# Kernel tuning notes

Hardware: AMD Instinct MI355X
Metric: run time of the kernel (lower is better)

## Reference

```python
import jax, jax.numpy as jnp
from jax import lax
import numpy as np

N_WORDS, SENT_LEN, N_HEADS = 8192, 64, 1024
INPUT_SIZE, HIDDEN, DIST_EMB, CONV_CH, MAX_DIST = 768, 1024, 64, 4, 128
L_MAX = SENT_LEN  # static max sentence length (uniform sentences in setup)


def setup_inputs():
    key = jax.random.key(0)
    ks = jax.random.split(key, 8)
    sent_id = (jnp.arange(N_WORDS) // SENT_LEN).astype(jnp.int32)
    words = jax.random.normal(ks[0], (N_WORDS, INPUT_SIZE), jnp.float32)
    heads_ids = jnp.sort(jax.random.randint(ks[1], (N_HEADS,), 0, N_WORDS)).astype(jnp.int32)
    in_dim = 2 * INPUT_SIZE + DIST_EMB
    def lin(k, i, o):
        return (jax.random.normal(k, (i, o), jnp.float32) / np.float32(np.sqrt(i)))
    return dict(
        sent_id=sent_id, words=words, heads_ids=heads_ids,
        W1=lin(ks[2], in_dim, HIDDEN), b1=jnp.zeros((HIDDEN,), jnp.float32),
        W2=lin(ks[3], HIDDEN, 256), b2=jnp.zeros((256,), jnp.float32),
        W3=lin(ks[4], 256, DIST_EMB), b3=jnp.zeros((DIST_EMB,), jnp.float32),
        conv1_w=jax.random.normal(ks[5], (CONV_CH, DIST_EMB, 3), jnp.float32) * 0.05,
        conv1_b=jnp.zeros((CONV_CH,), jnp.float32),
        conv2_w=jax.random.normal(ks[6], (2, CONV_CH, 3), jnp.float32) * 0.2,
        conv2_b=jnp.zeros((2,), jnp.float32),
        emb=jax.random.normal(ks[7], (MAX_DIST, DIST_EMB), jnp.float32),
    )


def _conv1d(x, w, b):
    # x: [N, C_in, L], w: [C_out, C_in, K=3]; padding=1 exactly as the torch module
    y = lax.conv_general_dilated(x, w, (1,), [(1, 1)],
                                 dimension_numbers=('NCH', 'OIH', 'NCH'))
    return y + b[None, :, None]


def reference(sent_id, words, heads_ids, W1, b1, W2, b2, W3, b3,
              conv1_w, conv1_b, conv2_w, conv2_b, emb):
    n_words = words.shape[0]
    n_heads = heads_ids.shape[0]
    md = emb.shape[0]
    heads = heads_ids.astype(jnp.int32)
    sid_h = sent_id[heads]
    # sent_id is sorted: each sentence is a contiguous run of words, so the
    # ragged nonzero(same_sent) cols for head h are start[h] .. start[h]+len[h]-1
    start = jnp.searchsorted(sent_id, sid_h, side='left')
    lengths = jnp.searchsorted(sent_id, sid_h, side='right') - start
    j = jnp.arange(L_MAX)
    cols = start[:, None] + j[None, :]                  # [H, L]
    valid = j[None, :] < lengths[:, None]               # padding_mask
    cols_c = jnp.minimum(cols, n_words - 1)
    rel = heads[:, None] - cols_c                       # relative positions
    emb_ids = rel + (md - 2) // 2
    emb_ids = jnp.where((emb_ids < 0) | (emb_ids > md - 2), md - 1, emb_ids)
    # padded pair matrix: [H, L, 2*input + dist_emb], zeros at padded slots
    pair = jnp.concatenate([
        jnp.broadcast_to(words[heads][:, None, :], (n_heads, L_MAX, words.shape[1])),
        words[cols_c],
        emb[emb_ids],
    ], axis=-1)
    pair = jnp.where(valid[..., None], pair, 0.0)
    # FFNN (eval mode: dropout = identity)
    h = jax.nn.relu(pair @ W1 + b1)
    h = jax.nn.relu(h @ W2 + b2)
    h = h @ W3 + b3                                     # [H, L, DIST_EMB]
    x = jnp.transpose(h, (0, 2, 1))                     # [H, C, L]
    x = _conv1d(x, conv1_w, conv1_b)
    x = _conv1d(x, conv2_w, conv2_b)
    res = jnp.transpose(x, (0, 2, 1))                   # [H, L, 2]
    # scatter valid entries back into a -inf-filled [H, n_words, 2] tensor
    scores = jnp.full((n_heads, n_words, 2), -jnp.inf, jnp.float32)
    rows = jnp.broadcast_to(jnp.arange(n_heads)[:, None], cols.shape)
    cols_sc = jnp.where(valid, cols, n_words)           # OOB index -> dropped
    scores = scores.at[rows, cols_sc].set(res, mode='drop')
    # eval-mode validity masks: starts must be <= head, ends >= head
    rel_full = heads[:, None] - jnp.arange(n_words)[None, :]
    valid_starts = jnp.where(rel_full >= 0, 0.0, -jnp.inf)
    valid_ends = jnp.where(rel_full <= 0, 0.0, -jnp.inf)
    return scores + jnp.stack([valid_starts, valid_ends], axis=2)
```

## Files before the change

kernel.cpp:

```cpp
#include <hip/hip_runtime.h>
#include <cstdint>
#include <cstddef>

#define NW   8192
#define NH   1024
#define INP  768
#define HID  1024
#define DE   64
#define LMAX 64

#define NEG_SENT (-3.0e38f)

typedef short bf16x8 __attribute__((ext_vector_type(8)));
typedef float f32x4  __attribute__((ext_vector_type(4)));

__device__ __forceinline__ unsigned short f2bf(float f) {
    unsigned u = __builtin_bit_cast(unsigned, f);
    u += 0x7FFFu + ((u >> 16) & 1u);
    return (unsigned short)(u >> 16);
}
__device__ __forceinline__ float bcf(unsigned u) {
    return __builtin_bit_cast(float, u);
}

__device__ __forceinline__ void gload_lds16(const void* g, void* lds) {
    __builtin_amdgcn_global_load_lds(
        (const __attribute__((address_space(1))) unsigned int*)g,
        (__attribute__((address_space(3))) unsigned int*)lds, 16, 0, 0);
}

__device__ __forceinline__ bf16x8 mk_af(uint4 u, uint4 v, uint4 e) {
    bf16x8 r;
    const unsigned* up = (const unsigned*)&u;
    const unsigned* vp = (const unsigned*)&v;
    const unsigned* ep = (const unsigned*)&e;
    unsigned* rp = (unsigned*)&r;
    #pragma unroll
    for (int q = 0; q < 4; ++q) {
        const unsigned ud = up[q], vd = vp[q], ed = ep[q];
        float slo = bcf(ud << 16) + bcf(vd << 16) + bcf(ed << 16);
        float shi = bcf(ud & 0xffff0000u) + bcf(vd & 0xffff0000u) + bcf(ed & 0xffff0000u);
        slo = fmaxf(slo, 0.f);
        shi = fmaxf(shi, 0.f);
        rp[q] = (unsigned)f2bf(slo) | ((unsigned)f2bf(shi) << 16);
    }
    return r;
}

__device__ __forceinline__ bf16x8 cvt8(float4 x, float4 y) {
    bf16x8 r;
    r[0] = (short)f2bf(x.x); r[1] = (short)f2bf(x.y);
    r[2] = (short)f2bf(x.z); r[3] = (short)f2bf(x.w);
    r[4] = (short)f2bf(y.x); r[5] = (short)f2bf(y.y);
    r[6] = (short)f2bf(y.z); r[7] = (short)f2bf(y.w);
    return r;
}

__device__ __forceinline__ void pack_frags_body(
    const float* __restrict__ src, uint4* __restrict__ dst,
    int Ntiles, int N, int t)
{
    const int frag = t >> 6, l = t & 63;
    const int kc = frag / Ntiles, nt = frag - kc * Ntiles;
    const int k0 = kc * 32 + ((l >> 4) << 3);
    const int n  = nt * 16 + (l & 15);
    unsigned wv[4];
    #pragma unroll
    for (int r = 0; r < 4; ++r) {
        const unsigned lo = f2bf(src[(size_t)(k0 + 2 * r)     * N + n]);
        const unsigned hi = f2bf(src[(size_t)(k0 + 2 * r + 1) * N + n]);
        wv[r] = lo | (hi << 16);
    }
    dst[t] = make_uint4(wv[0], wv[1], wv[2], wv[3]);
}

__global__ __launch_bounds__(256) void pack_all(
    const int* __restrict__ sent_id, const int* __restrict__ heads_ids,
    const float* __restrict__ W1, const float* __restrict__ b1,
    const float* __restrict__ W2, const float* __restrict__ W3,
    uint4* __restrict__ W2p, uint4* __restrict__ W3p,
    uint4* __restrict__ W1bp, uint4* __restrict__ W1ap,
    uint4* __restrict__ W1cp,
    unsigned short* __restrict__ b1b, unsigned short* __restrict__ zrow,
    int* __restrict__ hstart, int* __restrict__ hlen)
{
    const int b = blockIdx.x, tid = threadIdx.x;
    if (b < 4) {
        const int i = b * 256 + tid;
        b1b[i] = f2bf(b1[i]);
        zrow[i] = 0;
        const int head = heads_ids[i];
        const int sid = sent_id[head];
        int lo = 0, hi = NW;
        while (lo < hi) { int m = (lo + hi) >> 1; if (sent_id[m] < sid) lo = m + 1; else hi = m; }
        const int st = lo;
        int lo2 = lo, hi2 = NW;
        while (lo2 < hi2) { int m = (lo2 + hi2) >> 1; if (sent_id[m] <= sid) lo2 = m + 1; else hi2 = m; }
        int ln = lo2 - st;
        if (ln > LMAX) ln = LMAX;
        hstart[i] = st; hlen[i] = ln;
    }
    else if (b < 132)  pack_frags_body(W2, W2p, 16, 256, (b - 4) * 256 + tid);
    else if (b < 140)  pack_frags_body(W3, W3p, 4, 64, (b - 132) * 256 + tid);
    else if (b < 524)  pack_frags_body(W1 + (size_t)INP * HID, W1bp, 64, 1024, (b - 140) * 256 + tid);
    else if (b < 908)  pack_frags_body(W1, W1ap, 64, 1024, (b - 524) * 256 + tid);
    else               pack_frags_body(W1 + (size_t)2 * INP * HID, W1cp, 64, 1024, (b - 908) * 256 + tid);
}

__global__ __launch_bounds__(256) void gemm_vue(
    const float* __restrict__ words, const int* __restrict__ heads_ids,
    const float* __restrict__ emb,
    const uint4* __restrict__ W1bp, const uint4* __restrict__ W1ap,
    const uint4* __restrict__ W1cp, const float* __restrict__ b1,
    unsigned short* __restrict__ Vb, unsigned short* __restrict__ Ub,
    unsigned short* __restrict__ Eb)
{
    __shared__ char sbuf[2][16384];
    const int tid = threadIdx.x;
    const int l = tid & 63, wid = tid >> 6;

    const float* Asrc; const int* gather = nullptr;
    const uint4* Bp; unsigned short* Cb; const float* bias = nullptr;
    int Kc, by, bx, lda;
    {
        const int bid = blockIdx.x;
        if (bid < 512)      { Asrc = words; lda = INP; Bp = W1bp; Cb = Vb; Kc = 24; by = bid >> 3; bx = bid & 7; }
        else if (bid < 576) { const int bb = bid - 512; Asrc = words; lda = INP; gather = heads_ids; Bp = W1ap; Cb = Ub; bias = b1; Kc = 24; by = bb >> 3; bx = bb & 7; }
        else                { const int bb = bid - 576; Asrc = emb; lda = DE; Bp = W1cp; Cb = Eb; Kc = 2; by = 0; bx = bb; }
    }
    const int mt0 = by * 8, nt0 = bx * 8;
    const int NtTot = 64, N = 1024;
    const int wm = (wid >> 1) * 4, wn = (wid & 1) * 4;

    const float* arow[2]; int koffA[2];
    #pragma unroll
    for (int q = 0; q < 2; ++q) {
        const int e = tid + q * 256;
        const int f = e >> 6, ll2 = e & 63;
        int r = (mt0 + f) * 16 + (ll2 & 15);
        if (gather) r = gather[r];
        arow[q]  = Asrc + (size_t)r * lda;
        koffA[q] = (ll2 >> 4) << 3;
    }

    f32x4 acc[4][4];
    #pragma unroll
    for (int i = 0; i < 4; ++i)
        #pragma unroll
        for (int j = 0; j < 4; ++j) acc[i][j] = (f32x4){0.f, 0.f, 0.f, 0.f};

    float4 a0, a1, a2, a3;
    #define STAGE_A_LOAD(kc) do {                                          \
        a0 = *(const float4*)(arow[0] + (kc) * 32 + koffA[0]);             \
        a1 = *(const float4*)(arow[0] + (kc) * 32 + koffA[0] + 4);         \
        a2 = *(const float4*)(arow[1] + (kc) * 32 + koffA[1]);             \
        a3 = *(const float4*)(arow[1] + (kc) * 32 + koffA[1] + 4); } while (0)
    #define STAGE_B(kc, b) do {                                            \
        gload_lds16(Bp + ((size_t)(kc) * NtTot + nt0 + wid) * 64 + l,      \
                    sbuf[b] + 8192 + wid * 1024 + l * 16);                 \
        gload_lds16(Bp + ((size_t)(kc) * NtTot + nt0 + 4 + wid) * 64 + l,  \
                    sbuf[b] + 8192 + (4 + wid) * 1024 + l * 16); } while (0)
    #define STAGE_A_WRITE(b) do {                                          \
        *(bf16x8*)(sbuf[b] + tid * 16)         = cvt8(a0, a1);             \
        *(bf16x8*)(sbuf[b] + (tid + 256) * 16) = cvt8(a2, a3); } while (0)

    STAGE_A_LOAD(0);
    STAGE_B(0, 0);
    STAGE_A_WRITE(0);

    for (int kc = 0; kc < Kc; ++kc) {
        const int p = kc & 1;
        __builtin_amdgcn_s_barrier();
        if (kc + 1 < Kc) {
            STAGE_A_LOAD(kc + 1);
            STAGE_B(kc + 1, p ^ 1);
            STAGE_A_WRITE(p ^ 1);
            asm volatile("s_waitcnt vmcnt(2) lgkmcnt(0)" ::: "memory");
        } else {
            asm volatile("s_waitcnt vmcnt(0) lgkmcnt(0)" ::: "memory");
        }
        __builtin_amdgcn_s_barrier();
        bf16x8 af[4], bf[4];
        #pragma unroll
        for (int i = 0; i < 4; ++i)
            af[i] = *(const bf16x8*)(sbuf[p] + ((wm + i) * 64 + l) * 16);
        #pragma unroll
        for (int j = 0; j < 4; ++j)
            bf[j] = *(const bf16x8*)(sbuf[p] + 8192 + ((wn + j) * 64 + l) * 16);
        #pragma unroll
        for (int i = 0; i < 4; ++i)
            #pragma unroll
            for (int j = 0; j < 4; ++j)
                acc[i][j] = __builtin_amdgcn_mfma_f32_16x16x32_bf16(
                    af[i], bf[j], acc[i][j], 0, 0, 0);
    }
    #undef STAGE_A_LOAD
    #undef STAGE_B
    #undef STAGE_A_WRITE

    const int bm = mt0 * 16, bn = nt0 * 16;
    #pragma unroll
    for (int i = 0; i < 4; ++i)
        #pragma unroll
        for (int j = 0; j < 4; ++j) {
            const int row0 = bm + (wm + i) * 16 + ((l >> 4) << 2);
            const int col  = bn + (wn + j) * 16 + (l & 15);
            const float bv = bias ? bias[col] : 0.f;
            #pragma unroll
            for (int r = 0; r < 4; ++r)
                Cb[(size_t)(row0 + r) * N + col] = f2bf(acc[i][j][r] + bv);
        }
}

__global__ __launch_bounds__(256, 4) void head_kernel(
    const int* __restrict__ hstart, const int* __restrict__ hlen,
    const int* __restrict__ heads_ids,
    const unsigned short* __restrict__ Vb, const unsigned short* __restrict__ Ub,
    const unsigned short* __restrict__ Eb, const unsigned short* __restrict__ b1b,
    const unsigned short* __restrict__ zrow,
    const uint4* __restrict__ W2p, const float* __restrict__ b2,
    const uint4* __restrict__ W3p, const float* __restrict__ b3,
    const float* __restrict__ c1w, const float* __restrict__ c1b,
    const float* __restrict__ c2w, const float* __restrict__ c2b,
    float* __restrict__ out)
{
    __shared__ char smem[32768];
    const int h   = (blockIdx.x & 7) * 128 + (blockIdx.x >> 3);
    const int tid = threadIdx.x;
    const int w = tid >> 6, l = tid & 63;
    const int head  = heads_ids[h];
    const int start = hstart[h];
    const int len   = hlen[h];

    const int arow = w * 16 + (l & 15);
    const int g8   = (l >> 4) << 3;
    const bool valid = arow < len;
    const int wglob = start + arow;
    const int wc    = wglob < NW ? wglob : NW - 1;
    int eid = head - wc + 63;
    eid = (eid < 0 || eid > 126) ? 127 : eid;
    const unsigned short* Vp = valid ? Vb + (size_t)wc  * HID : zrow;
    const unsigned short* Ep = valid ? Eb + (size_t)eid * HID : zrow;

    if (tid < 128)
        *(uint4*)(smem + 8192 + tid * 16) = *(const uint4*)(Ub + (size_t)h * HID + tid * 8);
    else
        *(uint4*)(smem + 10240 + (tid - 128) * 16) = *(const uint4*)(b1b + (tid - 128) * 8);
    const char* ubase = smem + (valid ? 8192 : 10240);

    char* slot0 = smem;
    char* slot1 = smem + 4096;
    const uint4* WpB = W2p + (size_t)(w * 4) * 64 + l;

    f32x4 acc[16];
    #pragma unroll
    for (int i = 0; i < 16; ++i) acc[i] = (f32x4){0.f, 0.f, 0.f, 0.f};

    uint4 vX, eX, vY, eY;
    bf16x8 Ba0, Ba1, Ba2, Ba3;

    #define LOAD_VE(kc, vv, ee) do {                           \
        vv = *(const uint4*)(Vp + (kc) * 32 + g8);             \
        ee = *(const uint4*)(Ep + (kc) * 32 + g8); } while (0)
    #define LOAD_U(kc) (*(const uint4*)(ubase + (kc) * 64 + (g8 << 1)))
    #define LOAD_B(kc) do {                                    \
        const uint4* p_ = WpB + (size_t)(kc) * 16 * 64;        \
        Ba0 = *(const bf16x8*)(p_);                            \
        Ba1 = *(const bf16x8*)(p_ + 64);                       \
        Ba2 = *(const bf16x8*)(p_ + 128);                      \
        Ba3 = *(const bf16x8*)(p_ + 192); } while (0)
    #define CONSUME(slot) do {                                 \
        bf16x8 a0 = *(const bf16x8*)((slot) + 0 * 1024 + l * 16); \
        bf16x8 a1 = *(const bf16x8*)((slot) + 1 * 1024 + l * 16); \
        bf16x8 a2 = *(const bf16x8*)((slot) + 2 * 1024 + l * 16); \
        bf16x8 a3 = *(const bf16x8*)((slot) + 3 * 1024 + l * 16); \
        acc[0]  = __builtin_amdgcn_mfma_f32_16x16x32_bf16(a0, Ba0, acc[0],  0,0,0); \
        acc[1]  = __builtin_amdgcn_mfma_f32_16x16x32_bf16(a0, Ba1, acc[1],  0,0,0); \
        acc[2]  = __builtin_amdgcn_mfma_f32_16x16x32_bf16(a0, Ba2, acc[2],  0,0,0); \
        acc[3]  = __builtin_amdgcn_mfma_f32_16x16x32_bf16(a0, Ba3, acc[3],  0,0,0); \
        acc[4]  = __builtin_amdgcn_mfma_f32_16x16x32_bf16(a1, Ba0, acc[4],  0,0,0); \
        acc[5]  = __builtin_amdgcn_mfma_f32_16x16x32_bf16(a1, Ba1, acc[5],  0,0,0); \
        acc[6]  = __builtin_amdgcn_mfma_f32_16x16x32_bf16(a1, Ba2, acc[6],  0,0,0); \
        acc[7]  = __builtin_amdgcn_mfma_f32_16x16x32_bf16(a1, Ba3, acc[7],  0,0,0); \
        acc[8]  = __builtin_amdgcn_mfma_f32_16x16x32_bf16(a2, Ba0, acc[8],  0,0,0); \
        acc[9]  = __builtin_amdgcn_mfma_f32_16x16x32_bf16(a2, Ba1, acc[9],  0,0,0); \
        acc[10] = __builtin_amdgcn_mfma_f32_16x16x32_bf16(a2, Ba2, acc[10], 0,0,0); \
        acc[11] = __builtin_amdgcn_mfma_f32_16x16x32_bf16(a2, Ba3, acc[11], 0,0,0); \
        acc[12] = __builtin_amdgcn_mfma_f32_16x16x32_bf16(a3, Ba0, acc[12], 0,0,0); \
        acc[13] = __builtin_amdgcn_mfma_f32_16x16x32_bf16(a3, Ba1, acc[13], 0,0,0); \
        acc[14] = __builtin_amdgcn_mfma_f32_16x16x32_bf16(a3, Ba2, acc[14], 0,0,0); \
        acc[15] = __builtin_amdgcn_mfma_f32_16x16x32_bf16(a3, Ba3, acc[15], 0,0,0); } while (0)

    LOAD_VE(0, vX, eX);
    LOAD_VE(1, vY, eY);
    LOAD_B(0);
    __syncthreads();
    {
        bf16x8 af = mk_af(LOAD_U(0), vX, eX);
        *(bf16x8*)(slot0 + w * 1024 + l * 16) = af;
    }
    LOAD_VE(2, vX, eX);

    for (int kc = 0; kc < 32; kc += 2) {
        asm volatile("s_waitcnt lgkmcnt(0)" ::: "memory");
        __builtin_amdgcn_s_barrier();
        {
            bf16x8 af = mk_af(LOAD_U(kc + 1), vY, eY);
            *(bf16x8*)(slot1 + w * 1024 + l * 16) = af;
        }
        if (kc + 3 < 32) LOAD_VE(kc + 3, vY, eY);
        CONSUME(slot0);
        LOAD_B(kc + 1);
        asm volatile("s_waitcnt lgkmcnt(0)" ::: "memory");
        __builtin_amdgcn_s_barrier();
        if (kc + 2 < 32) {
            bf16x8 af = mk_af(LOAD_U(kc + 2), vX, eX);
            *(bf16x8*)(slot0 + w * 1024 + l * 16) = af;
        }
        if (kc + 4 < 32) LOAD_VE(kc + 4, vX, eX);
        CONSUME(slot1);
        if (kc + 2 < 32) LOAD_B(kc + 2);
    }
    #undef LOAD_VE
    #undef LOAD_U
    #undef LOAD_B
    #undef CONSUME

    __syncthreads();
    {
        float b2v[4];
        #pragma unroll
        for (int ntl = 0; ntl < 4; ++ntl) b2v[ntl] = b2[w * 64 + ntl * 16 + (l & 15)];
        #pragma unroll
        for (int mt = 0; mt < 4; ++mt)
            #pragma unroll
            for (int ntl = 0; ntl < 4; ++ntl) {
                const int n = w * 64 + ntl * 16 + (l & 15);
                #pragma unroll
                for (int r = 0; r < 4; ++r) {
                    const int m = mt * 16 + ((l >> 4) << 2) + r;
                    const float x = fmaxf(acc[mt * 4 + ntl][r] + b2v[ntl], 0.f);
                    *(unsigned short*)(smem + m * 512 + ((n * 2) ^ ((m & 7) << 4))) = f2bf(x);
                }
            }
    }
    __syncthreads();

    f32x4 acc3[4];
    #pragma unroll
    for (int i = 0; i < 4; ++i) acc3[i] = (f32x4){0.f, 0.f, 0.f, 0.f};
    const int mrow = w * 16 + (l & 15);
    #pragma unroll
    for (int kc = 0; kc < 8; ++kc) {
        const int n0 = kc * 32 + g8;
        const bf16x8 af = *(const bf16x8*)(smem + mrow * 512 + ((n0 * 2) ^ ((mrow & 7) << 4)));
        #pragma unroll
        for (int nt = 0; nt < 4; ++nt) {
            const bf16x8 bf = *(const bf16x8*)(W3p + (size_t)((kc << 2) + nt) * 64 + l);
            acc3[nt] = __builtin_amdgcn_mfma_f32_16x16x32_bf16(af, bf, acc3[nt], 0, 0, 0);
        }
    }
    __syncthreads();
    float* h3s = (float*)smem;
    float* o1  = (float*)(smem + 16640);
    #pragma unroll
    for (int nt = 0; nt < 4; ++nt) {
        const int c = nt * 16 + (l & 15);
        const float b3v = b3[c];
        #pragma unroll
        for (int r = 0; r < 4; ++r) {
            const int m = w * 16 + ((l >> 4) << 2) + r;
            h3s[m * 65 + c] = acc3[nt][r] + b3v;
        }
    }
    if (tid < 8) o1[(tid >> 1) * 66 + ((tid & 1) ? 65 : 0)] = 0.f;
    __syncthreads();

    {
        const int o = tid >> 6, ll = tid & 63;
        float a = c1b[o];
        #pragma unroll 8
        for (int cc = 0; cc < 64; ++cc) {
            const float w0  = c1w[o * 192 + cc * 3 + 0];
            const float w1  = c1w[o * 192 + cc * 3 + 1];
            const float w2v = c1w[o * 192 + cc * 3 + 2];
            if (ll > 0)  a += h3s[(ll - 1) * 65 + cc] * w0;
            a += h3s[ll * 65 + cc] * w1;
            if (ll < 63) a += h3s[(ll + 1) * 65 + cc] * w2v;
        }
        o1[o * 66 + ll + 1] = a;
    }
    __syncthreads();

    if (tid < 128) {
        const int s = tid >> 6, ll = tid & 63;
        float z = c2b[s];
        #pragma unroll
        for (int cc = 0; cc < 4; ++cc)
            #pragma unroll
            for (int k = 0; k < 3; ++k)
                z += o1[cc * 66 + ll + k] * c2w[s * 12 + cc * 3 + k];
        if (ll < len) {
            const int wv = start + ll;
            const bool ok = (s == 0) ? (wv <= head) : (wv >= head);
            out[(size_t)h * (NW * 2) + (size_t)wv * 2 + s] = ok ? z : NEG_SENT;
        }
    }

    {
        float4 ni; ni.x = NEG_SENT; ni.y = NEG_SENT; ni.z = NEG_SENT; ni.w = NEG_SENT;
        float4* orow = reinterpret_cast<float4*>(out + (size_t)h * (NW * 2));
        const int cA = start >> 1;
        const int cB = (start + len - 1) >> 1;
        for (int ch = tid; ch < NW / 2; ch += 256) {
            if (ch >= cA && ch <= cB) {
                #pragma unroll
                for (int t = 0; t < 2; ++t) {
                    const int wv = 2 * ch + t;
                    if (wv < start || wv >= start + len) {
                        out[(size_t)h * (NW * 2) + (size_t)wv * 2]     = NEG_SENT;
                        out[(size_t)h * (NW * 2) + (size_t)wv * 2 + 1] = NEG_SENT;
                    }
                }
            } else {
                orow[ch] = ni;
            }
        }
    }
}

extern "C" void kernel_launch(void* const* d_in, const int* in_sizes, int n_in,
                              void* d_out, int out_size, void* d_ws, size_t ws_size,
                              hipStream_t stream)
{
    const int*   sent_id = (const int*)  d_in[0];
    const float* words   = (const float*)d_in[1];
    const int*   heads   = (const int*)  d_in[2];
    const float* W1      = (const float*)d_in[3];
    const float* b1      = (const float*)d_in[4];
    const float* W2      = (const float*)d_in[5];
    const float* b2      = (const float*)d_in[6];
    const float* W3      = (const float*)d_in[7];
    const float* b3      = (const float*)d_in[8];
    const float* c1w     = (const float*)d_in[9];
    const float* c1b     = (const float*)d_in[10];
    const float* c2w     = (const float*)d_in[11];
    const float* c2b     = (const float*)d_in[12];
    const float* emb     = (const float*)d_in[13];
    float* out = (float*)d_out;

    uint4* W2p  = (uint4*)d_ws;
    uint4* W3p  = W2p  + 32 * 16 * 64;
    uint4* W1bp = W3p  + 8 * 4 * 64;
    uint4* W1ap = W1bp + 24 * 64 * 64;
    uint4* W1cp = W1ap + 24 * 64 * 64;
    unsigned short* Vb   = (unsigned short*)(W1cp + 2 * 64 * 64);
    unsigned short* Ub   = Vb + (size_t)NW * HID;
    unsigned short* Eb   = Ub + (size_t)NH * HID;
    unsigned short* b1b  = Eb + (size_t)128 * HID;
    unsigned short* zrow = b1b + HID;
    int* hstart = (int*)(zrow + HID);
    int* hlen   = hstart + NH;

    dim3 blk(256);
    pack_all<<<dim3(940), blk, 0, stream>>>(
        sent_id, heads, W1, b1, W2, W3,
        W2p, W3p, W1bp, W1ap, W1cp, b1b, zrow, hstart, hlen);
    gemm_vue<<<dim3(584), blk, 0, stream>>>(
        words, heads, emb, W1bp, W1ap, W1cp, b1, Vb, Ub, Eb);
    head_kernel<<<dim3(NH), blk, 0, stream>>>(
        hstart, hlen, heads, Vb, Ub, Eb, b1b, zrow,
        W2p, b2, W3p, b3, c1w, c1b, c2w, c2b, out);
}
```

Measured before the change: 227.8 us.

## Pre-pack activations to bf16 MFMA fragments and use hardware bf16 conversion

Moves the fp32-to-bf16 conversion of word, gathered-head and embedding rows out of the GEMM main loop into the packing kernel. Operands are written in MFMA fragment layout, so the GEMM can stream both A and B into LDS with direct global-to-LDS loads. Software round-to-nearest bf16 conversion is replaced everywhere by the v_cvt_pk_bf16_f32 instruction. In exchange it adds an extra full write and re-read of packed activations (about 12 MB of bf16 for words) through global memory, plus a larger pack launch.

Measured after the change: 211.3 us. 7.3% less time.

```diff
diff --git a/kernel.cpp b/kernel.cpp
--- a/kernel.cpp
+++ b/kernel.cpp
@@ -22,6 +22,11 @@
 __device__ __forceinline__ float bcf(unsigned u) {
     return __builtin_bit_cast(float, u);
 }
+__device__ __forceinline__ unsigned cvtpk(float a, float b) {
+    unsigned r;
+    asm("v_cvt_pk_bf16_f32 %0, %1, %2" : "=v"(r) : "v"(a), "v"(b));
+    return r;
+}
 
 __device__ __forceinline__ void gload_lds16(const void* g, void* lds) {
     __builtin_amdgcn_global_load_lds(
@@ -40,19 +45,8 @@
         const unsigned ud = up[q], vd = vp[q], ed = ep[q];
         float slo = bcf(ud << 16) + bcf(vd << 16) + bcf(ed << 16);
         float shi = bcf(ud & 0xffff0000u) + bcf(vd & 0xffff0000u) + bcf(ed & 0xffff0000u);
-        slo = fmaxf(slo, 0.f);
-        shi = fmaxf(shi, 0.f);
-        rp[q] = (unsigned)f2bf(slo) | ((unsigned)f2bf(shi) << 16);
-    }
-    return r;
-}
-
-__device__ __forceinline__ bf16x8 cvt8(float4 x, float4 y) {
-    bf16x8 r;
-    r[0] = (short)f2bf(x.x); r[1] = (short)f2bf(x.y);
-    r[2] = (short)f2bf(x.z); r[3] = (short)f2bf(x.w);
-    r[4] = (short)f2bf(y.x); r[5] = (short)f2bf(y.y);
-    r[6] = (short)f2bf(y.z); r[7] = (short)f2bf(y.w);
+        rp[q] = cvtpk(fmaxf(slo, 0.f), fmaxf(shi, 0.f));
+    }
     return r;
 }
 
@@ -66,11 +60,26 @@
     const int n  = nt * 16 + (l & 15);
     unsigned wv[4];
     #pragma unroll
-    for (int r = 0; r < 4; ++r) {
-        const unsigned lo = f2bf(src[(size_t)(k0 + 2 * r)     * N + n]);
-        const unsigned hi = f2bf(src[(size_t)(k0 + 2 * r + 1) * N + n]);
-        wv[r] = lo | (hi << 16);
-    }
+    for (int r = 0; r < 4; ++r)
+        wv[r] = cvtpk(src[(size_t)(k0 + 2 * r) * N + n],
+                      src[(size_t)(k0 + 2 * r + 1) * N + n]);
+    dst[t] = make_uint4(wv[0], wv[1], wv[2], wv[3]);
+}
+
+__device__ __forceinline__ void pack_rows_body(
+    const float* __restrict__ src, uint4* __restrict__ dst,
+    const int* __restrict__ gather, int Kc, int ldsrc, int t)
+{
+    const int l = t & 63, frag = t >> 6;
+    const int mt = frag / Kc, kc = frag - mt * Kc;
+    int row = mt * 16 + (l & 15);
+    if (gather) row = gather[row];
+    const int k0 = kc * 32 + ((l >> 4) << 3);
+    const float* s = src + (size_t)row * ldsrc + k0;
+    unsigned wv[4];
+    #pragma unroll
+    for (int r = 0; r < 4; ++r)
+        wv[r] = cvtpk(s[2 * r], s[2 * r + 1]);
     dst[t] = make_uint4(wv[0], wv[1], wv[2], wv[3]);
 }
 
@@ -78,9 +87,11 @@
     const int* __restrict__ sent_id, const int* __restrict__ heads_ids,
     const float* __restrict__ W1, const float* __restrict__ b1,
     const float* __restrict__ W2, const float* __restrict__ W3,
+    const float* __restrict__ words, const float* __restrict__ emb,
     uint4* __restrict__ W2p, uint4* __restrict__ W3p,
     uint4* __restrict__ W1bp, uint4* __restrict__ W1ap,
-    uint4* __restrict__ W1cp,
+    uint4* __restrict__ W1cp, uint4* __restrict__ Ep_a,
+    uint4* __restrict__ Awp, uint4* __restrict__ Aup,
     unsigned short* __restrict__ b1b, unsigned short* __restrict__ zrow,
     int* __restrict__ hstart, int* __restrict__ hlen)
 {
@@ -104,89 +115,75 @@
     else if (b < 140)  pack_frags_body(W3, W3p, 4, 64, (b - 132) * 256 + tid);
     else if (b < 524)  pack_frags_body(W1 + (size_t)INP * HID, W1bp, 64, 1024, (b - 140) * 256 + tid);
     else if (b < 908)  pack_frags_body(W1, W1ap, 64, 1024, (b - 524) * 256 + tid);
-    else               pack_frags_body(W1 + (size_t)2 * INP * HID, W1cp, 64, 1024, (b - 908) * 256 + tid);
+    else if (b < 940)  pack_frags_body(W1 + (size_t)2 * INP * HID, W1cp, 64, 1024, (b - 908) * 256 + tid);
+    else if (b < 4012) pack_rows_body(words, Awp, nullptr, 24, INP, (b - 940) * 256 + tid);
+    else if (b < 4396) pack_rows_body(words, Aup, heads_ids, 24, INP, (b - 4012) * 256 + tid);
+    else               pack_rows_body(emb, Ep_a, nullptr, 2, DE, (b - 4396) * 256 + tid);
 }
 
 __global__ __launch_bounds__(256) void gemm_vue(
-    const float* __restrict__ words, const int* __restrict__ heads_ids,
-    const float* __restrict__ emb,
-    const uint4* __restrict__ W1bp, const uint4* __restrict__ W1ap,
-    const uint4* __restrict__ W1cp, const float* __restrict__ b1,
+    const uint4* __restrict__ Awp, const uint4* __restrict__ W1bp,
+    const uint4* __restrict__ Aup, const uint4* __restrict__ W1ap,
+    const uint4* __restrict__ Ep_a, const uint4* __restrict__ W1cp,
+    const float* __restrict__ b1,
     unsigned short* __restrict__ Vb, unsigned short* __restrict__ Ub,
     unsigned short* __restrict__ Eb)
 {
-    __shared__ char sbuf[2][16384];
+    __shared__ uint4 sAB[2][1024];
     const int tid = threadIdx.x;
     const int l = tid & 63, wid = tid >> 6;
 
-    const float* Asrc; const int* gather = nullptr;
-    const uint4* Bp; unsigned short* Cb; const float* bias = nullptr;
-    int Kc, by, bx, lda;
+    const uint4 *Ap, *Bp;
+    unsigned short* Cb;
+    const float* bias = nullptr;
+    int Kc, by, bx;
     {
         const int bid = blockIdx.x;
-        if (bid < 512)      { Asrc = words; lda = INP; Bp = W1bp; Cb = Vb; Kc = 24; by = bid >> 3; bx = bid & 7; }
-        else if (bid < 576) { const int bb = bid - 512; Asrc = words; lda = INP; gather = heads_ids; Bp = W1ap; Cb = Ub; bias = b1; Kc = 24; by = bb >> 3; bx = bb & 7; }
-        else                { const int bb = bid - 576; Asrc = emb; lda = DE; Bp = W1cp; Cb = Eb; Kc = 2; by = 0; bx = bb; }
+        if (bid < 512)      { Ap = Awp;  Bp = W1bp; Cb = Vb; Kc = 24; by = bid >> 3; bx = bid & 7; }
+        else if (bid < 576) { const int bb = bid - 512; Ap = Aup; Bp = W1ap; Cb = Ub; bias = b1; Kc = 24; by = bb >> 3; bx = bb & 7; }
+        else                { const int bb = bid - 576; Ap = Ep_a; Bp = W1cp; Cb = Eb; Kc = 2; by = 0; bx = bb; }
     }
     const int mt0 = by * 8, nt0 = bx * 8;
     const int NtTot = 64, N = 1024;
     const int wm = (wid >> 1) * 4, wn = (wid & 1) * 4;
 
-    const float* arow[2]; int koffA[2];
-    #pragma unroll
-    for (int q = 0; q < 2; ++q) {
-        const int e = tid + q * 256;
-        const int f = e >> 6, ll2 = e & 63;
-        int r = (mt0 + f) * 16 + (ll2 & 15);
-        if (gather) r = gather[r];
-        arow[q]  = Asrc + (size_t)r * lda;
-        koffA[q] = (ll2 >> 4) << 3;
-    }
-
     f32x4 acc[4][4];
     #pragma unroll
     for (int i = 0; i < 4; ++i)
         #pragma unroll
         for (int j = 0; j < 4; ++j) acc[i][j] = (f32x4){0.f, 0.f, 0.f, 0.f};
 
-    float4 a0, a1, a2, a3;
-    #define STAGE_A_LOAD(kc) do {                                          \
-        a0 = *(const float4*)(arow[0] + (kc) * 32 + koffA[0]);             \
-        a1 = *(const float4*)(arow[0] + (kc) * 32 + koffA[0] + 4);         \
-        a2 = *(const float4*)(arow[1] + (kc) * 32 + koffA[1]);             \
-        a3 = *(const float4*)(arow[1] + (kc) * 32 + koffA[1] + 4); } while (0)
-    #define STAGE_B(kc, b) do {                                            \
-        gload_lds16(Bp + ((size_t)(kc) * NtTot + nt0 + wid) * 64 + l,      \
-                    sbuf[b] + 8192 + wid * 1024 + l * 16);                 \
-        gload_lds16(Bp + ((size_t)(kc) * NtTot + nt0 + 4 + wid) * 64 + l,  \
-                    sbuf[b] + 8192 + (4 + wid) * 1024 + l * 16); } while (0)
-    #define STAGE_A_WRITE(b) do {                                          \
-        *(bf16x8*)(sbuf[b] + tid * 16)         = cvt8(a0, a1);             \
-        *(bf16x8*)(sbuf[b] + (tid + 256) * 16) = cvt8(a2, a3); } while (0)
-
-    STAGE_A_LOAD(0);
-    STAGE_B(0, 0);
-    STAGE_A_WRITE(0);
+    #pragma unroll
+    for (int i = 0; i < 2; ++i) {
+        const int f = i * 4 + wid;
+        gload_lds16(Ap + (size_t)(mt0 + f) * Kc * 64 + l, &sAB[0][f * 64 + l]);
+        gload_lds16(Bp + (size_t)(nt0 + f) * 64 + l,      &sAB[0][(8 + f) * 64 + l]);
+    }
 
     for (int kc = 0; kc < Kc; ++kc) {
         const int p = kc & 1;
         __builtin_amdgcn_s_barrier();
         if (kc + 1 < Kc) {
-            STAGE_A_LOAD(kc + 1);
-            STAGE_B(kc + 1, p ^ 1);
-            STAGE_A_WRITE(p ^ 1);
-            asm volatile("s_waitcnt vmcnt(2) lgkmcnt(0)" ::: "memory");
+            #pragma unroll
+            for (int i = 0; i < 2; ++i) {
+                const int f = i * 4 + wid;
+                gload_lds16(Ap + ((size_t)(mt0 + f) * Kc + kc + 1) * 64 + l,
+                            &sAB[p ^ 1][f * 64 + l]);
+                gload_lds16(Bp + ((size_t)(kc + 1) * NtTot + nt0 + f) * 64 + l,
+                            &sAB[p ^ 1][(8 + f) * 64 + l]);
+            }
+            asm volatile("s_waitcnt vmcnt(4)" ::: "memory");
         } else {
-            asm volatile("s_waitcnt vmcnt(0) lgkmcnt(0)" ::: "memory");
+            asm volatile("s_waitcnt vmcnt(0)" ::: "memory");
         }
         __builtin_amdgcn_s_barrier();
         bf16x8 af[4], bf[4];
         #pragma unroll
         for (int i = 0; i < 4; ++i)
-            af[i] = *(const bf16x8*)(sbuf[p] + ((wm + i) * 64 + l) * 16);
+            af[i] = *(const bf16x8*)&sAB[p][(wm + i) * 64 + l];
         #pragma unroll
         for (int j = 0; j < 4; ++j)
-            bf[j] = *(const bf16x8*)(sbuf[p] + 8192 + ((wn + j) * 64 + l) * 16);
+            bf[j] = *(const bf16x8*)&sAB[p][(8 + wn + j) * 64 + l];
         #pragma unroll
         for (int i = 0; i < 4; ++i)
             #pragma unroll
@@ -194,9 +191,6 @@
                 acc[i][j] = __builtin_amdgcn_mfma_f32_16x16x32_bf16(
                     af[i], bf[j], acc[i][j], 0, 0, 0);
     }
-    #undef STAGE_A_LOAD
-    #undef STAGE_B
-    #undef STAGE_A_WRITE
 
     const int bm = mt0 * 16, bn = nt0 * 16;
     #pragma unroll
@@ -206,9 +200,12 @@
             const int row0 = bm + (wm + i) * 16 + ((l >> 4) << 2);
             const int col  = bn + (wn + j) * 16 + (l & 15);
             const float bv = bias ? bias[col] : 0.f;
-            #pragma unroll
-            for (int r = 0; r < 4; ++r)
-                Cb[(size_t)(row0 + r) * N + col] = f2bf(acc[i][j][r] + bv);
+            const unsigned pA = cvtpk(acc[i][j][0] + bv, acc[i][j][1] + bv);
+            const unsigned pB = cvtpk(acc[i][j][2] + bv, acc[i][j][3] + bv);
+            Cb[(size_t)(row0 + 0) * N + col] = (unsigned short)pA;
+            Cb[(size_t)(row0 + 1) * N + col] = (unsigned short)(pA >> 16);
+            Cb[(size_t)(row0 + 2) * N + col] = (unsigned short)pB;
+            Cb[(size_t)(row0 + 3) * N + col] = (unsigned short)(pB >> 16);
         }
 }
 
@@ -336,12 +333,16 @@
             #pragma unroll
             for (int ntl = 0; ntl < 4; ++ntl) {
                 const int n = w * 64 + ntl * 16 + (l & 15);
-                #pragma unroll
-                for (int r = 0; r < 4; ++r) {
-                    const int m = mt * 16 + ((l >> 4) << 2) + r;
-                    const float x = fmaxf(acc[mt * 4 + ntl][r] + b2v[ntl], 0.f);
-                    *(unsigned short*)(smem + m * 512 + ((n * 2) ^ ((m & 7) << 4))) = f2bf(x);
-                }
+                const int m0 = mt * 16 + ((l >> 4) << 2);
+                const f32x4 a = acc[mt * 4 + ntl];
+                const unsigned pA = cvtpk(fmaxf(a[0] + b2v[ntl], 0.f),
+                                          fmaxf(a[1] + b2v[ntl], 0.f));
+                const unsigned pB = cvtpk(fmaxf(a[2] + b2v[ntl], 0.f),
+                                          fmaxf(a[3] + b2v[ntl], 0.f));
+                *(unsigned short*)(smem + (m0 + 0) * 512 + ((n * 2) ^ (((m0 + 0) & 7) << 4))) = (unsigned short)pA;
+                *(unsigned short*)(smem + (m0 + 1) * 512 + ((n * 2) ^ (((m0 + 1) & 7) << 4))) = (unsigned short)(pA >> 16);
+                *(unsigned short*)(smem + (m0 + 2) * 512 + ((n * 2) ^ (((m0 + 2) & 7) << 4))) = (unsigned short)pB;
+                *(unsigned short*)(smem + (m0 + 3) * 512 + ((n * 2) ^ (((m0 + 3) & 7) << 4))) = (unsigned short)(pB >> 16);
             }
     }
     __syncthreads();
@@ -454,7 +455,10 @@
     uint4* W1bp = W3p  + 8 * 4 * 64;
     uint4* W1ap = W1bp + 24 * 64 * 64;
     uint4* W1cp = W1ap + 24 * 64 * 64;
-    unsigned short* Vb   = (unsigned short*)(W1cp + 2 * 64 * 64);
+    uint4* Ep_a = W1cp + 2 * 64 * 64;
+    uint4* Awp  = Ep_a + 8 * 2 * 64;
+    uint4* Aup  = Awp  + 512 * 24 * 64;
+    unsigned short* Vb   = (unsigned short*)(Aup + 64 * 24 * 64);
     unsigned short* Ub   = Vb + (size_t)NW * HID;
     unsigned short* Eb   = Ub + (size_t)NH * HID;
     unsigned short* b1b  = Eb + (size_t)128 * HID;
@@ -463,11 +467,11 @@
     int* hlen   = hstart + NH;
 
     dim3 blk(256);
-    pack_all<<<dim3(940), blk, 0, stream>>>(
-        sent_id, heads, W1, b1, W2, W3,
-        W2p, W3p, W1bp, W1ap, W1cp, b1b, zrow, hstart, hlen);
+    pack_all<<<dim3(4400), blk, 0, stream>>>(
+        sent_id, heads, W1, b1, W2, W3, words, emb,
+        W2p, W3p, W1bp, W1ap, W1cp, Ep_a, Awp, Aup, b1b, zrow, hstart, hlen);
     gemm_vue<<<dim3(584), blk, 0, stream>>>(
-        words, heads, emb, W1bp, W1ap, W1cp, b1, Vb, Ub, Eb);
+        Awp, W1bp, Aup, W1ap, Ep_a, W1cp, b1, Vb, Ub, Eb);
     head_kernel<<<dim3(NH), blk, 0, stream>>>(
         hstart, hlen, heads, Vb, Ub, Eb, b1b, zrow,
         W2p, b2, W3p, b3, c1w, c1b, c2w, c2b, out);
```
